# Kernel optimization log

Hardware: AMD Instinct MI355X
Metric: run time of the kernel (lower is better)

Reference implementation:

```python
import jax, jax.numpy as jnp
import numpy as np

N = 100000
E = 1600000


def setup_inputs() -> dict:
    key = jax.random.key(0)
    ks = jax.random.split(key, 8)
    x = jax.random.normal(ks[0], (N, 4), dtype=jnp.float32)
    edge_index = jax.random.randint(ks[1], (2, E), 0, N)
    # Glorot-ish scaled weights
    W1 = jax.random.normal(ks[2], (4, 64), dtype=jnp.float32) / np.sqrt(4.0)
    b1 = jnp.zeros((64,), dtype=jnp.float32)
    W2 = jax.random.normal(ks[3], (64, 32), dtype=jnp.float32) / np.sqrt(64.0)
    b2 = jnp.zeros((32,), dtype=jnp.float32)
    Wf = jax.random.normal(ks[4], (32, 32), dtype=jnp.float32) / np.sqrt(32.0)
    bf = jnp.zeros((32,), dtype=jnp.float32)
    return {"x": x, "edge_index": edge_index, "W1": W1, "b1": b1,
            "W2": W2, "b2": b2, "Wf": Wf, "bf": bf}


def _gcn_conv(x, W, b, src, dst, n):
    """PyG GCNConv: out = D^{-1/2}(A+I)D^{-1/2} (x @ W) + b, sum-aggregated at dst."""
    h = x @ W  # [n, out] -- linear before propagate, like PyG
    # degree over dst (self-loops already appended in src/dst)
    deg = jax.ops.segment_sum(jnp.ones_like(dst, dtype=h.dtype), dst, num_segments=n)
    dinv = jnp.where(deg > 0, jax.lax.rsqrt(jnp.maximum(deg, 1.0)), 0.0)
    norm = dinv[src] * dinv[dst]  # [E+n]
    msg = h[src] * norm[:, None]  # gather + scale
    out = jax.ops.segment_sum(msg, dst, num_segments=n)  # scatter-add
    return out + b


def reference(x, edge_index, W1, b1, W2, b2, Wf, bf):
    n = x.shape[0]
    loops = jnp.arange(n, dtype=edge_index.dtype)
    src = jnp.concatenate([edge_index[0], loops])
    dst = jnp.concatenate([edge_index[1], loops])
    h = jax.nn.relu(_gcn_conv(x, W1, b1, src, dst, n))
    h = jax.nn.relu(_gcn_conv(h, W2, b2, src, dst, n))
    return jax.nn.relu(h @ Wf + bf)
```

## Files before the change

kernel.cpp:

```cpp
#include <hip/hip_runtime.h>
#include <hip/hip_fp16.h>


#define STRIDE 64
#define BSHIFT 7
#define CH 8192
#define PBS 1024
#define PT (CH / PBS)

__global__ __launch_bounds__(PBS) void k_place(const int* __restrict__ src,
                                               const int* __restrict__ dst,
                                               int* __restrict__ gcur,
                                               int* __restrict__ ebuf,
                                               int NB, int CAP, int E) {
    __shared__ int stage[CH];
    __shared__ unsigned short stageb[CH];
    __shared__ int histA[1024];
    __shared__ int gbaseL[1024];
    __shared__ int wtot[16];
    const int tid = threadIdx.x;
    const int base = blockIdx.x * CH;
    const int blkcnt = min(CH, E - base);

    histA[tid] = 0;
    __syncthreads();

    int posr[PT];
    unsigned short bkr[PT];
    unsigned char lnr[PT];
#pragma unroll
    for (int k = 0; k < PT; ++k) {
        int e = base + tid + k * PBS;
        if (e < E) {
            int d = dst[e];
            int b = d >> BSHIFT;
            bkr[k] = (unsigned short)b;
            lnr[k] = (unsigned char)(d & 127);
            posr[k] = atomicAdd(&histA[b], 1);
        }
    }
    __syncthreads();

    {
        int lane = tid & 63, wid = tid >> 6;
        int v = histA[tid];
#pragma unroll
        for (int o = 1; o < 64; o <<= 1) {
            int t2 = __shfl_up(v, o, 64);
            if (lane >= o) v += t2;
        }
        if (lane == 63) wtot[wid] = v;
        __syncthreads();
        int wpre = 0;
        for (int ww = 0; ww < wid; ++ww) wpre += wtot[ww];
        histA[tid] = v + wpre;
    }
    __syncthreads();

    int* A = histA;

    if (tid < NB) {
        int st = tid ? A[tid - 1] : 0;
        int cnt = A[tid] - st;
        gbaseL[tid] = cnt ? atomicAdd(&gcur[tid], cnt) : 0;
    }
    __syncthreads();

#pragma unroll
    for (int k = 0; k < PT; ++k) {
        int e = base + tid + k * PBS;
        if (e < E) {
            int b = bkr[k];
            int st = b ? A[b - 1] : 0;
            int idx = st + posr[k];
            stage[idx] = src[e] | ((int)lnr[k] << 17);
            stageb[idx] = (unsigned short)b;
        }
    }
    __syncthreads();

    for (int j = tid; j < blkcnt; j += PBS) {
        int b = stageb[j];
        int st = b ? A[b - 1] : 0;
        int o = gbaseL[b] + (j - st);
        if (o < CAP) ebuf[(size_t)b * CAP + o] = stage[j];
    }
}

__global__ __launch_bounds__(512) void k_fillsorted2(const int* __restrict__ ebuf,
                                                     const int* __restrict__ gcur,
                                                     int* __restrict__ adjF,
                                                     int* __restrict__ deg,
                                                     float* __restrict__ dinv,
                                                     const float4* __restrict__ x,
                                                     float4* __restrict__ xd,
                                                     int CAP, int N) {
    __shared__ int adjL[128 * STRIDE];
    __shared__ int cnt[128];
    const int b = blockIdx.x, tid = threadIdx.x;
    for (int j = tid; j < 128 * (STRIDE / 4); j += 512)
        ((int4*)adjL)[j] = make_int4(0, 0, 0, 0);
    if (tid < 128) cnt[tid] = 0;
    __syncthreads();

    int count = min(gcur[b], CAP);
    const int* eb = ebuf + (size_t)b * CAP;
    for (int j = tid; j < count; j += 512) {
        int v = eb[j];
        int ln = (v >> 17) & 127;
        int s = v & 0x1FFFF;
        int slot = atomicAdd(&cnt[ln], 1);
        if (slot < STRIDE) adjL[(ln << 6) | slot] = s;
    }
    __syncthreads();

    const size_t gbase4 = (size_t)b << 11;
    for (int j4 = tid; j4 < 128 * (STRIDE / 4); j4 += 512) {
        int rowc = cnt[j4 >> 4];
        int q = j4 & 15;
        if (q < 8 || rowc > 32) ((int4*)adjF)[gbase4 + j4] = ((int4*)adjL)[j4];
    }

    if (tid < 128) {
        int node = (b << BSHIFT) + tid;
        if (node < N) {
            int k = cnt[tid];
            deg[node] = k;
            float di = rsqrtf((float)(k + 1));
            dinv[node] = di;
            float4 xv = x[node];
            xv.x *= di; xv.y *= di; xv.z *= di; xv.w *= di;
            xd[node] = xv;
        }
    }
}

__global__ __launch_bounds__(512) void k_aggmlp(const int* __restrict__ deg,
                                                const int* __restrict__ adjF,
                                                const float4* __restrict__ xd,
                                                const float* __restrict__ dinv,
                                                const float* __restrict__ W1,
                                                const float* __restrict__ b1,
                                                const float* __restrict__ W2,
                                                signed char* __restrict__ Qq,
                                                int n) {
    __shared__ float4 W2L[512];
    const int tid = threadIdx.x;
    W2L[tid] = ((const float4*)W2)[tid];

    const int lane = tid & 31;
    const int sub = lane >> 3;
    const int sl  = lane & 7;
    const int nib = (tid >> 5) * 4 + sub;
    const int node = blockIdx.x * 64 + nib;
    bool valid = node < n;
    int nd = valid ? node : 0;
    const int* row = adjF + ((size_t)nd << 6);

    int r0 = row[sl], r1 = row[sl + 8], r2 = row[sl + 16];
    int c = valid ? min(deg[nd], STRIDE) : 0;
    float4 self = xd[nd];
    float di = dinv[nd];
    float4 v0 = xd[r0];
    float4 v1 = xd[r1];
    float4 v2 = xd[r2];
    float m0 = (sl      < c) ? 1.0f : 0.0f;
    float m1 = (sl + 8  < c) ? 1.0f : 0.0f;
    float m2 = (sl + 16 < c) ? 1.0f : 0.0f;
    float ax = fmaf(m0, v0.x, fmaf(m1, v1.x, m2 * v2.x));
    float ay = fmaf(m0, v0.y, fmaf(m1, v1.y, m2 * v2.y));
    float az = fmaf(m0, v0.z, fmaf(m1, v1.z, m2 * v2.z));
    float aw = fmaf(m0, v0.w, fmaf(m1, v1.w, m2 * v2.w));

    for (int kk = 24 + sl; kk < c; kk += 8) {
        float4 v = xd[row[kk]];
        ax += v.x; ay += v.y; az += v.z; aw += v.w;
    }
#pragma unroll
    for (int m = 4; m >= 1; m >>= 1) {
        ax += __shfl_xor(ax, m, 8);
        ay += __shfl_xor(ay, m, 8);
        az += __shfl_xor(az, m, 8);
        aw += __shfl_xor(aw, m, 8);
    }

    float bx = (ax + self.x) * di, by = (ay + self.y) * di;
    float bz = (az + self.z) * di, bw = (aw + self.w) * di;

    __syncthreads();

    float q0 = 0.f, q1 = 0.f, q2 = 0.f, q3 = 0.f;
#pragma unroll 8
    for (int j = 0; j < 64; ++j) {
        float h = fmaf(bx, W1[j], fmaf(by, W1[64 + j],
                  fmaf(bz, W1[128 + j], fmaf(bw, W1[192 + j], b1[j]))));
        h = fmaxf(h, 0.0f);
        float4 wv = W2L[(j << 3) + sl];
        q0 = fmaf(h, wv.x, q0);
        q1 = fmaf(h, wv.y, q1);
        q2 = fmaf(h, wv.z, q2);
        q3 = fmaf(h, wv.w, q3);
    }
    q0 *= di; q1 *= di; q2 *= di; q3 *= di;
    float rm = fmaxf(fmaxf(fabsf(q0), fabsf(q1)), fmaxf(fabsf(q2), fabsf(q3)));
    rm = fmaxf(rm, 1e-12f);
#pragma unroll
    for (int m = 4; m >= 1; m >>= 1) rm = fmaxf(rm, __shfl_xor(rm, m, 8));
    float inv = 127.0f / rm;
    unsigned p0 = (unsigned)(__float2int_rn(q0 * inv)) & 0xFFu;
    unsigned p1 = (unsigned)(__float2int_rn(q1 * inv)) & 0xFFu;
    unsigned p2 = (unsigned)(__float2int_rn(q2 * inv)) & 0xFFu;
    unsigned p3 = (unsigned)(__float2int_rn(q3 * inv)) & 0xFFu;
    unsigned pk = p0 | (p1 << 8) | (p2 << 16) | (p3 << 24);
    if (valid) {
        signed char* qrow = Qq + ((size_t)nd << 6);
        ((unsigned*)qrow)[sl] = pk;
        if (sl == 0) *(float*)(qrow + 32) = rm * (1.0f / 127.0f);
    }
}

__global__ void k_final(const int* __restrict__ deg, const int* __restrict__ adjF,
                        const float* __restrict__ dinv,
                        const signed char* __restrict__ Qq,
                        const float* __restrict__ b2,
                        const float* __restrict__ Wf, const float* __restrict__ bf,
                        float* __restrict__ out, int n) {
    int node = blockIdx.x * (blockDim.x >> 5) + (threadIdx.x >> 5);
    int lane = threadIdx.x & 31;
    bool valid = node < n;
    int nd = valid ? node : 0;
    const int* row = adjF + ((size_t)nd << 6);
    const int nb = lane >> 3;
    const int cw = lane & 7;

    int s[6];
#pragma unroll
    for (int g = 0; g < 6; ++g) s[g] = row[(g << 2) + nb];

    int c = valid ? min(deg[nd], STRIDE) : 0;

    float di   = dinv[nd];
    float bb2  = b2[lane];
    float bbf  = bf[lane];
    const signed char* qsrow = Qq + ((size_t)nd << 6);
    float qself = *(const float*)(qsrow + 32) * (float)qsrow[lane];

    float a0 = 0.f, a1 = 0.f, a2 = 0.f, a3 = 0.f;
#pragma unroll
    for (int g = 0; g < 6; ++g) {
        const signed char* qrow = Qq + ((size_t)s[g] << 6);
        int wv = ((const int*)qrow)[cw];
        float sc = *(const float*)(qrow + 32);
        sc = ((g << 2) + nb < c) ? sc : 0.0f;
        a0 = fmaf(sc, (float)((signed char)(wv)), a0);
        a1 = fmaf(sc, (float)((signed char)(wv >> 8)), a1);
        a2 = fmaf(sc, (float)((signed char)(wv >> 16)), a2);
        a3 = fmaf(sc, (float)(wv >> 24), a3);
    }

    for (int k = 24; k < c; k += 16) {
        int i0 = k + nb, i1 = k + 4 + nb, i2 = k + 8 + nb, i3 = k + 12 + nb;
        int s0 = row[min(i0, c - 1)];
        int s1 = row[min(i1, c - 1)];
        int s2 = row[min(i2, c - 1)];
        int s3 = row[min(i3, c - 1)];
        const signed char* q0p = Qq + ((size_t)s0 << 6);
        const signed char* q1p = Qq + ((size_t)s1 << 6);
        const signed char* q2p = Qq + ((size_t)s2 << 6);
        const signed char* q3p = Qq + ((size_t)s3 << 6);
        int w0 = ((const int*)q0p)[cw];
        int w1 = ((const int*)q1p)[cw];
        int w2 = ((const int*)q2p)[cw];
        int w3 = ((const int*)q3p)[cw];
        float sc0 = *(const float*)(q0p + 32); sc0 = (i0 < c) ? sc0 : 0.0f;
        float sc1 = *(const float*)(q1p + 32); sc1 = (i1 < c) ? sc1 : 0.0f;
        float sc2 = *(const float*)(q2p + 32); sc2 = (i2 < c) ? sc2 : 0.0f;
        float sc3 = *(const float*)(q3p + 32); sc3 = (i3 < c) ? sc3 : 0.0f;
        a0 = fmaf(sc0, (float)((signed char)(w0)), a0);
        a1 = fmaf(sc0, (float)((signed char)(w0 >> 8)), a1);
        a2 = fmaf(sc0, (float)((signed char)(w0 >> 16)), a2);
        a3 = fmaf(sc0, (float)(w0 >> 24), a3);
        a0 = fmaf(sc1, (float)((signed char)(w1)), a0);
        a1 = fmaf(sc1, (float)((signed char)(w1 >> 8)), a1);
        a2 = fmaf(sc1, (float)((signed char)(w1 >> 16)), a2);
        a3 = fmaf(sc1, (float)(w1 >> 24), a3);
        a0 = fmaf(sc2, (float)((signed char)(w2)), a0);
        a1 = fmaf(sc2, (float)((signed char)(w2 >> 8)), a1);
        a2 = fmaf(sc2, (float)((signed char)(w2 >> 16)), a2);
        a3 = fmaf(sc2, (float)(w2 >> 24), a3);
        a0 = fmaf(sc3, (float)((signed char)(w3)), a0);
        a1 = fmaf(sc3, (float)((signed char)(w3 >> 8)), a1);
        a2 = fmaf(sc3, (float)((signed char)(w3 >> 16)), a2);
        a3 = fmaf(sc3, (float)(w3 >> 24), a3);
    }

    a0 += __shfl_xor(a0, 8, 32);  a0 += __shfl_xor(a0, 16, 32);
    a1 += __shfl_xor(a1, 8, 32);  a1 += __shfl_xor(a1, 16, 32);
    a2 += __shfl_xor(a2, 8, 32);  a2 += __shfl_xor(a2, 16, 32);
    a3 += __shfl_xor(a3, 8, 32);  a3 += __shfl_xor(a3, 16, 32);

    int srcl = lane >> 2;
    float t0 = __shfl(a0, srcl, 32);
    float t1 = __shfl(a1, srcl, 32);
    float t2 = __shfl(a2, srcl, 32);
    float t3 = __shfl(a3, srcl, 32);
    int r2 = lane & 3;
    float accv = (r2 & 1) ? t1 : t0;
    float hi   = (r2 & 1) ? t3 : t2;
    accv = (r2 & 2) ? hi : accv;

    accv += qself;

    float h = fmaxf(fmaf(accv, di, bb2), 0.0f);

    float o0 = bbf, o1 = 0.0f, o2 = 0.0f, o3 = 0.0f;
#pragma unroll
    for (int cc = 0; cc < 32; cc += 4) {
        o0 = fmaf(__shfl(h, cc + 0, 32), Wf[(cc + 0) * 32 + lane], o0);
        o1 = fmaf(__shfl(h, cc + 1, 32), Wf[(cc + 1) * 32 + lane], o1);
        o2 = fmaf(__shfl(h, cc + 2, 32), Wf[(cc + 2) * 32 + lane], o2);
        o3 = fmaf(__shfl(h, cc + 3, 32), Wf[(cc + 3) * 32 + lane], o3);
    }
    float o = (o0 + o1) + (o2 + o3);
    if (valid) out[((size_t)node << 5) | lane] = fmaxf(o, 0.0f);
}

static inline size_t align_up(size_t x, size_t a) { return (x + a - 1) & ~(a - 1); }

extern "C" void kernel_launch(void* const* d_in, const int* in_sizes, int n_in,
                              void* d_out, int out_size, void* d_ws, size_t ws_size,
                              hipStream_t stream) {
    const int N = in_sizes[0] / 4;
    const int E = in_sizes[1] / 2;

    const float* x  = (const float*)d_in[0];
    const int*   ei = (const int*)d_in[1];
    const int*   src = ei;
    const int*   dst = ei + E;
    const float* W1 = (const float*)d_in[2];
    const float* b1 = (const float*)d_in[3];
    const float* W2 = (const float*)d_in[4];
    const float* b2 = (const float*)d_in[5];
    const float* Wf = (const float*)d_in[6];
    const float* bf = (const float*)d_in[7];
    float* out = (float*)d_out;

    const int NB  = (N + 127) >> BSHIFT;
    const int CAP = ((E + NB - 1) / NB) * 5 / 4 + 64;

    char* w = (char*)d_ws;
    size_t off = 0;
    int*    gcur = (int*)(w + off);         off += align_up((size_t)NB * 4, 256);
    int*    deg  = (int*)(w + off);         off += align_up((size_t)N * 4, 256);
    float*  dinv = (float*)(w + off);       off += align_up((size_t)N * 4, 256);
    float*  xd   = (float*)(w + off);       off += align_up((size_t)N * 16, 256);
    int*    adjF = (int*)(w + off);         off += align_up((size_t)NB * 128 * STRIDE * 4, 256);
    signed char* Qq = (signed char*)(w + off); off += align_up((size_t)N * 64, 256);
    int*    ebuf = (int*)(w + off);         off += align_up((size_t)NB * CAP * 4, 256);

    const int B = 256;
    const int nplace = (E + CH - 1) / CH;

    hipMemsetAsync(gcur, 0, (size_t)NB * 4, stream);
    k_place<<<nplace, PBS, 0, stream>>>(src, dst, gcur, ebuf, NB, CAP, E);
    k_fillsorted2<<<NB, 512, 0, stream>>>(ebuf, gcur, adjF, deg, dinv,
                                          (const float4*)x, (float4*)xd, CAP, N);
    k_aggmlp<<<(N + 63) / 64, 512, 0, stream>>>(deg, adjF, (const float4*)xd,
                                                dinv, W1, b1, W2, Qq, N);
    k_final<<<((size_t)N * 32 + B - 1) / B, B, 0, stream>>>(deg, adjF, dinv, Qq,
                                                            b2, Wf, bf, out, N);
}
```

Before: 147.6 us.

## Replace two-pass bucketed adjacency build with direct global atomic scatter

Removes the block-local bucket sort (k_place) and the per-bucket LDS compaction (k_fillsorted2). In their place, a single kernel does a global atomicAdd on deg[dst] and writes src straight into a fixed 64-slot adjacency row, followed by a small per-node prep kernel for dinv and xd. This drops the ebuf staging buffer and one pass over the edges. In exchange it relies on random global atomics and scattered writes, and it needs a full memset of the adjacency array, which the old path avoided by writing only 32 slots for low-degree rows.

```diff
diff --git a/kernel.cpp b/kernel.cpp
--- a/kernel.cpp
+++ b/kernel.cpp
@@ -3,135 +3,29 @@
 
 
 #define STRIDE 64
-#define BSHIFT 7
-#define CH 8192
-#define PBS 1024
-#define PT (CH / PBS)
-
-__global__ __launch_bounds__(PBS) void k_place(const int* __restrict__ src,
-                                               const int* __restrict__ dst,
-                                               int* __restrict__ gcur,
-                                               int* __restrict__ ebuf,
-                                               int NB, int CAP, int E) {
-    __shared__ int stage[CH];
-    __shared__ unsigned short stageb[CH];
-    __shared__ int histA[1024];
-    __shared__ int gbaseL[1024];
-    __shared__ int wtot[16];
-    const int tid = threadIdx.x;
-    const int base = blockIdx.x * CH;
-    const int blkcnt = min(CH, E - base);
-
-    histA[tid] = 0;
-    __syncthreads();
-
-    int posr[PT];
-    unsigned short bkr[PT];
-    unsigned char lnr[PT];
-#pragma unroll
-    for (int k = 0; k < PT; ++k) {
-        int e = base + tid + k * PBS;
-        if (e < E) {
-            int d = dst[e];
-            int b = d >> BSHIFT;
-            bkr[k] = (unsigned short)b;
-            lnr[k] = (unsigned char)(d & 127);
-            posr[k] = atomicAdd(&histA[b], 1);
-        }
-    }
-    __syncthreads();
-
-    {
-        int lane = tid & 63, wid = tid >> 6;
-        int v = histA[tid];
-#pragma unroll
-        for (int o = 1; o < 64; o <<= 1) {
-            int t2 = __shfl_up(v, o, 64);
-            if (lane >= o) v += t2;
-        }
-        if (lane == 63) wtot[wid] = v;
-        __syncthreads();
-        int wpre = 0;
-        for (int ww = 0; ww < wid; ++ww) wpre += wtot[ww];
-        histA[tid] = v + wpre;
-    }
-    __syncthreads();
-
-    int* A = histA;
-
-    if (tid < NB) {
-        int st = tid ? A[tid - 1] : 0;
-        int cnt = A[tid] - st;
-        gbaseL[tid] = cnt ? atomicAdd(&gcur[tid], cnt) : 0;
-    }
-    __syncthreads();
-
-#pragma unroll
-    for (int k = 0; k < PT; ++k) {
-        int e = base + tid + k * PBS;
-        if (e < E) {
-            int b = bkr[k];
-            int st = b ? A[b - 1] : 0;
-            int idx = st + posr[k];
-            stage[idx] = src[e] | ((int)lnr[k] << 17);
-            stageb[idx] = (unsigned short)b;
-        }
-    }
-    __syncthreads();
-
-    for (int j = tid; j < blkcnt; j += PBS) {
-        int b = stageb[j];
-        int st = b ? A[b - 1] : 0;
-        int o = gbaseL[b] + (j - st);
-        if (o < CAP) ebuf[(size_t)b * CAP + o] = stage[j];
-    }
-}
-
-__global__ __launch_bounds__(512) void k_fillsorted2(const int* __restrict__ ebuf,
-                                                     const int* __restrict__ gcur,
-                                                     int* __restrict__ adjF,
-                                                     int* __restrict__ deg,
-                                                     float* __restrict__ dinv,
-                                                     const float4* __restrict__ x,
-                                                     float4* __restrict__ xd,
-                                                     int CAP, int N) {
-    __shared__ int adjL[128 * STRIDE];
-    __shared__ int cnt[128];
-    const int b = blockIdx.x, tid = threadIdx.x;
-    for (int j = tid; j < 128 * (STRIDE / 4); j += 512)
-        ((int4*)adjL)[j] = make_int4(0, 0, 0, 0);
-    if (tid < 128) cnt[tid] = 0;
-    __syncthreads();
-
-    int count = min(gcur[b], CAP);
-    const int* eb = ebuf + (size_t)b * CAP;
-    for (int j = tid; j < count; j += 512) {
-        int v = eb[j];
-        int ln = (v >> 17) & 127;
-        int s = v & 0x1FFFF;
-        int slot = atomicAdd(&cnt[ln], 1);
-        if (slot < STRIDE) adjL[(ln << 6) | slot] = s;
-    }
-    __syncthreads();
-
-    const size_t gbase4 = (size_t)b << 11;
-    for (int j4 = tid; j4 < 128 * (STRIDE / 4); j4 += 512) {
-        int rowc = cnt[j4 >> 4];
-        int q = j4 & 15;
-        if (q < 8 || rowc > 32) ((int4*)adjF)[gbase4 + j4] = ((int4*)adjL)[j4];
-    }
-
-    if (tid < 128) {
-        int node = (b << BSHIFT) + tid;
-        if (node < N) {
-            int k = cnt[tid];
-            deg[node] = k;
-            float di = rsqrtf((float)(k + 1));
-            dinv[node] = di;
-            float4 xv = x[node];
-            xv.x *= di; xv.y *= di; xv.z *= di; xv.w *= di;
-            xd[node] = xv;
-        }
+
+__global__ void k_scatter(const int* __restrict__ src, const int* __restrict__ dst,
+                          int* __restrict__ deg, int* __restrict__ adjF, int E) {
+    int i = blockIdx.x * blockDim.x + threadIdx.x;
+    int stride = gridDim.x * blockDim.x;
+    for (int e = i; e < E; e += stride) {
+        int d = dst[e];
+        int s = src[e];
+        int slot = atomicAdd(&deg[d], 1);
+        if (slot < STRIDE) adjF[((size_t)d << 6) | slot] = s;
+    }
+}
+
+__global__ void k_prep(const int* __restrict__ deg, float* __restrict__ dinv,
+                       const float4* __restrict__ x, float4* __restrict__ xd, int N) {
+    int i = blockIdx.x * blockDim.x + threadIdx.x;
+    if (i < N) {
+        int k = deg[i];
+        float di = rsqrtf((float)(k + 1));
+        dinv[i] = di;
+        float4 xv = x[i];
+        xv.x *= di; xv.y *= di; xv.z *= di; xv.w *= di;
+        xd[i] = xv;
     }
 }
 
@@ -345,26 +239,22 @@
     const float* bf = (const float*)d_in[7];
     float* out = (float*)d_out;
 
-    const int NB  = (N + 127) >> BSHIFT;
-    const int CAP = ((E + NB - 1) / NB) * 5 / 4 + 64;
-
     char* w = (char*)d_ws;
     size_t off = 0;
-    int*    gcur = (int*)(w + off);         off += align_up((size_t)NB * 4, 256);
     int*    deg  = (int*)(w + off);         off += align_up((size_t)N * 4, 256);
     float*  dinv = (float*)(w + off);       off += align_up((size_t)N * 4, 256);
     float*  xd   = (float*)(w + off);       off += align_up((size_t)N * 16, 256);
-    int*    adjF = (int*)(w + off);         off += align_up((size_t)NB * 128 * STRIDE * 4, 256);
+    int*    adjF = (int*)(w + off);         off += align_up((size_t)N * STRIDE * 4, 256);
     signed char* Qq = (signed char*)(w + off); off += align_up((size_t)N * 64, 256);
-    int*    ebuf = (int*)(w + off);         off += align_up((size_t)NB * CAP * 4, 256);
 
     const int B = 256;
-    const int nplace = (E + CH - 1) / CH;
-
-    hipMemsetAsync(gcur, 0, (size_t)NB * 4, stream);
-    k_place<<<nplace, PBS, 0, stream>>>(src, dst, gcur, ebuf, NB, CAP, E);
-    k_fillsorted2<<<NB, 512, 0, stream>>>(ebuf, gcur, adjF, deg, dinv,
-                                          (const float4*)x, (float4*)xd, CAP, N);
+
+    hipMemsetAsync(deg, 0, (size_t)N * 4, stream);
+    hipMemsetAsync(adjF, 0, (size_t)N * STRIDE * 4, stream);
+    int nscat = min((E + B - 1) / B, 2048);
+    k_scatter<<<nscat, B, 0, stream>>>(src, dst, deg, adjF, E);
+    k_prep<<<(N + B - 1) / B, B, 0, stream>>>(deg, dinv, (const float4*)x,
+                                              (float4*)xd, N);
     k_aggmlp<<<(N + 63) / 64, 512, 0, stream>>>(deg, adjF, (const float4*)xd,
                                                 dinv, W1, b1, W2, Qq, N);
     k_final<<<((size_t)N * 32 + B - 1) / B, B, 0, stream>>>(deg, adjF, dinv, Qq,
```

New measurement: 256.3 us. 1.74x slower.
